# Kernel tuning notes

Hardware: AMD Instinct MI355X
Metric: run time of the kernel (lower is better)

## Reference

```python
import jax, jax.numpy as jnp
import numpy as np

EPS = 1e-6

def setup_inputs() -> dict:
    key = jax.random.key(0)
    k1, k2 = jax.random.split(key)
    N, B, T, D = 12, 4, 2048, 768
    layer_outputs = jax.random.normal(k1, (N, B, T, D), dtype=jnp.float32)
    pseudo_query = jax.random.normal(k2, (D,), dtype=jnp.float32) * 0.02
    key_norm_weight = jnp.ones((D,), dtype=jnp.float32)
    return {"layer_outputs": layer_outputs, "pseudo_query": pseudo_query,
            "key_norm_weight": key_norm_weight}

def reference(layer_outputs, pseudo_query, key_norm_weight):
    # layer_outputs: [N, B, T, D] (stacked V)
    V = layer_outputs
    # RMSNorm over last dim with learned scale
    inv_rms = jax.lax.rsqrt(jnp.mean(V * V, axis=-1, keepdims=True) + EPS)
    K = V * inv_rms * key_norm_weight  # [N,B,T,D]
    logits = jnp.einsum('d,nbtd->nbt', pseudo_query, K)  # [N,B,T]
    alpha = jax.nn.softmax(logits, axis=0)               # softmax over layer dim
    h = jnp.einsum('nbt,nbtd->btd', alpha, V)            # [B,T,D]
    return h
```

## Files before the change

### kernel.cpp

```cpp
#include <hip/hip_runtime.h>
#include <math.h>


constexpr int N_LAYERS = 12;
constexpr int D = 768;
constexpr int THREADS = 192;
constexpr float EPS = 1e-6f;

template<int CTRL>
__device__ __forceinline__ float dpp_add(float x) {
    int y = __builtin_amdgcn_update_dpp(0, __builtin_bit_cast(int, x),
                                        CTRL, 0xf, 0xf, false);
    return x + __builtin_bit_cast(float, y);
}

__device__ __forceinline__ float wave_sum_uniform(float x) {
    x = dpp_add<0x111>(x);
    x = dpp_add<0x112>(x);
    x = dpp_add<0x114>(x);
    x = dpp_add<0x118>(x);
    x = dpp_add<0x142>(x);
    x = dpp_add<0x143>(x);
    return __builtin_bit_cast(float,
        __builtin_amdgcn_readlane(__builtin_bit_cast(int, x), 63));
}

__global__ __launch_bounds__(THREADS)
void attnres_fused_kernel(const float* __restrict__ V,
                          const float* __restrict__ q,
                          const float* __restrict__ w,
                          float* __restrict__ out,
                          int BT)
{
    const int bt   = blockIdx.x;
    const int tid  = threadIdx.x;
    const int lane = tid & 63;
    const int wave = tid >> 6;

    const int d0 = tid * 4;
    float4 q4 = *reinterpret_cast<const float4*>(q + d0);
    float4 w4 = *reinterpret_cast<const float4*>(w + d0);
    float4 qw = make_float4(q4.x * w4.x, q4.y * w4.y, q4.z * w4.z, q4.w * w4.w);

    const size_t stride_n = (size_t)BT * (size_t)D;
    const float* base = V + (size_t)bt * (size_t)D + d0;

    float4 v[N_LAYERS];
    #pragma unroll
    for (int n = 0; n < N_LAYERS; ++n) {
        v[n] = *reinterpret_cast<const float4*>(base + (size_t)n * stride_n);
    }

    float ss[N_LAYERS], dq[N_LAYERS];
    #pragma unroll
    for (int n = 0; n < N_LAYERS; ++n) {
        float4 x = v[n];
        ss[n] = x.x * x.x + x.y * x.y + x.z * x.z + x.w * x.w;
        dq[n] = qw.x * x.x + qw.y * x.y + qw.z * x.z + qw.w * x.w;
    }

    float wred[2 * N_LAYERS];
    #pragma unroll
    for (int n = 0; n < N_LAYERS; ++n) {
        wred[n]            = wave_sum_uniform(ss[n]);
        wred[N_LAYERS + n] = wave_sum_uniform(dq[n]);
    }

    __shared__ float red[3][2 * N_LAYERS];
    if (lane == 0) {
        #pragma unroll
        for (int i = 0; i < 6; ++i) {
            *reinterpret_cast<float4*>(&red[wave][i * 4]) =
                make_float4(wred[i * 4 + 0], wred[i * 4 + 1],
                            wred[i * 4 + 2], wred[i * 4 + 3]);
        }
    }
    __syncthreads();

    float tot[2 * N_LAYERS];
    #pragma unroll
    for (int i = 0; i < 6; ++i) {
        float4 a = *reinterpret_cast<const float4*>(&red[0][i * 4]);
        float4 b = *reinterpret_cast<const float4*>(&red[1][i * 4]);
        float4 c = *reinterpret_cast<const float4*>(&red[2][i * 4]);
        tot[i * 4 + 0] = a.x + b.x + c.x;
        tot[i * 4 + 1] = a.y + b.y + c.y;
        tot[i * 4 + 2] = a.z + b.z + c.z;
        tot[i * 4 + 3] = a.w + b.w + c.w;
    }

    float logits[N_LAYERS];
    float mx = -3.0e38f;
    #pragma unroll
    for (int n = 0; n < N_LAYERS; ++n) {
        float inv_rms = rsqrtf(tot[n] * (1.0f / (float)D) + EPS);
        logits[n] = tot[N_LAYERS + n] * inv_rms;
        mx = fmaxf(mx, logits[n]);
    }
    float alpha[N_LAYERS];
    float sum = 0.0f;
    #pragma unroll
    for (int n = 0; n < N_LAYERS; ++n) {
        alpha[n] = __expf(logits[n] - mx);
        sum += alpha[n];
    }
    const float inv_sum = 1.0f / sum;

    float4 h = make_float4(0.f, 0.f, 0.f, 0.f);
    #pragma unroll
    for (int n = 0; n < N_LAYERS; ++n) {
        float a = alpha[n] * inv_sum;
        h.x += a * v[n].x;
        h.y += a * v[n].y;
        h.z += a * v[n].z;
        h.w += a * v[n].w;
    }

    *reinterpret_cast<float4*>(out + (size_t)bt * (size_t)D + d0) = h;
}

extern "C" void kernel_launch(void* const* d_in, const int* in_sizes, int n_in,
                              void* d_out, int out_size, void* d_ws, size_t ws_size,
                              hipStream_t stream)
{
    const float* V = (const float*)d_in[0];
    const float* q = (const float*)d_in[1];
    const float* w = (const float*)d_in[2];
    float* out = (float*)d_out;

    const int BT = out_size / D;

    attnres_fused_kernel<<<dim3(BT), dim3(THREADS), 0, stream>>>(V, q, w, out, BT);
}
```

Before: 60.78 us.

## Process multiple rows per block with double-buffered loads and bf16 value stash

Each block now handles eight token rows, alternating two register buffers so the next row's global loads are issued before the current row's reductions and barrier. Values used for the final weighted sum are packed to bf16 to reduce register pressure from the double buffers. The cross-wave reduction uses a double-buffered shared array and a raw barrier. The cost is lower precision in the output accumulation and fewer blocks in flight.

```diff
diff --git a/kernel.cpp b/kernel.cpp
--- a/kernel.cpp
+++ b/kernel.cpp
@@ -2,9 +2,10 @@
 #include <math.h>
 
 
-constexpr int N_LAYERS = 12;
+constexpr int NL = 12;
 constexpr int D = 768;
 constexpr int THREADS = 192;
+constexpr int PER = 8;
 constexpr float EPS = 1e-6f;
 
 template<int CTRL>
@@ -13,110 +14,138 @@
                                         CTRL, 0xf, 0xf, false);
     return x + __builtin_bit_cast(float, y);
 }
-
-__device__ __forceinline__ float wave_sum_uniform(float x) {
+__device__ __forceinline__ float wave_sum63(float x) {
     x = dpp_add<0x111>(x);
     x = dpp_add<0x112>(x);
     x = dpp_add<0x114>(x);
     x = dpp_add<0x118>(x);
     x = dpp_add<0x142>(x);
     x = dpp_add<0x143>(x);
-    return __builtin_bit_cast(float,
-        __builtin_amdgcn_readlane(__builtin_bit_cast(int, x), 63));
+    return x;
+}
+
+__device__ __forceinline__ unsigned pack_bf16x2(float a, float b) {
+    unsigned ua = __builtin_bit_cast(unsigned, a);
+    unsigned ub = __builtin_bit_cast(unsigned, b);
+    return ((ua + 0x8000u) >> 16) | ((ub + 0x8000u) & 0xFFFF0000u);
 }
 
 __global__ __launch_bounds__(THREADS)
-void attnres_fused_kernel(const float* __restrict__ V,
-                          const float* __restrict__ q,
-                          const float* __restrict__ w,
-                          float* __restrict__ out,
-                          int BT)
+void attnres_kernel(const float* __restrict__ V,
+                    const float* __restrict__ q,
+                    const float* __restrict__ w,
+                    float* __restrict__ out,
+                    int BT)
 {
-    const int bt   = blockIdx.x;
     const int tid  = threadIdx.x;
     const int lane = tid & 63;
     const int wave = tid >> 6;
+    const int d0   = tid * 4;
+    const int bt_base = blockIdx.x * PER;
 
-    const int d0 = tid * 4;
     float4 q4 = *reinterpret_cast<const float4*>(q + d0);
     float4 w4 = *reinterpret_cast<const float4*>(w + d0);
-    float4 qw = make_float4(q4.x * w4.x, q4.y * w4.y, q4.z * w4.z, q4.w * w4.w);
+    const float4 qw = make_float4(q4.x * w4.x, q4.y * w4.y,
+                                  q4.z * w4.z, q4.w * w4.w);
 
     const size_t stride_n = (size_t)BT * (size_t)D;
-    const float* base = V + (size_t)bt * (size_t)D + d0;
 
-    float4 v[N_LAYERS];
-    #pragma unroll
-    for (int n = 0; n < N_LAYERS; ++n) {
-        v[n] = *reinterpret_cast<const float4*>(base + (size_t)n * stride_n);
+    __shared__ float red[2][3][2 * NL];
+
+    float4   vA[NL],      vB[NL];
+    float    ssA[NL],     ssB[NL];
+    float    dqA[NL],     dqB[NL];
+    unsigned cA[2 * NL],  cB[2 * NL];
+
+    auto load_rows = [&](float4 (&v)[NL], int bt) {
+        const int btc = bt < BT ? bt : BT - 1;
+        const float* base = V + (size_t)btc * (size_t)D + d0;
+        #pragma unroll
+        for (int n = 0; n < NL; ++n)
+            v[n] = *reinterpret_cast<const float4*>(base + (size_t)n * stride_n);
+    };
+
+    auto ssdq_pack = [&](const float4 (&v)[NL], float (&ss)[NL],
+                         float (&dq)[NL], unsigned (&c)[2 * NL]) {
+        #pragma unroll
+        for (int n = 0; n < NL; ++n) {
+            const float4 x = v[n];
+            ss[n] = x.x * x.x + x.y * x.y + x.z * x.z + x.w * x.w;
+            dq[n] = qw.x * x.x + qw.y * x.y + qw.z * x.z + qw.w * x.w;
+            c[2 * n + 0] = pack_bf16x2(x.x, x.y);
+            c[2 * n + 1] = pack_bf16x2(x.z, x.w);
+        }
+    };
+
+    auto finish = [&](float (&ss)[NL], float (&dq)[NL],
+                      const unsigned (&c)[2 * NL], int bt, int p) {
+        float r[2 * NL];
+        #pragma unroll
+        for (int n = 0; n < NL; ++n) {
+            r[n]      = wave_sum63(ss[n]);
+            r[NL + n] = wave_sum63(dq[n]);
+        }
+        if (lane == 63) {
+            #pragma unroll
+            for (int i6 = 0; i6 < 6; ++i6)
+                *reinterpret_cast<float4*>(&red[p][wave][4 * i6]) =
+                    make_float4(r[4 * i6 + 0], r[4 * i6 + 1],
+                                r[4 * i6 + 2], r[4 * i6 + 3]);
+        }
+        __builtin_amdgcn_sched_barrier(0);
+        asm volatile("s_waitcnt lgkmcnt(0)");
+        __builtin_amdgcn_s_barrier();
+        __builtin_amdgcn_sched_barrier(0);
+
+        float tot[2 * NL];
+        #pragma unroll
+        for (int i6 = 0; i6 < 6; ++i6) {
+            float4 a  = *reinterpret_cast<const float4*>(&red[p][0][4 * i6]);
+            float4 b  = *reinterpret_cast<const float4*>(&red[p][1][4 * i6]);
+            float4 cc = *reinterpret_cast<const float4*>(&red[p][2][4 * i6]);
+            tot[4 * i6 + 0] = a.x + b.x + cc.x;
+            tot[4 * i6 + 1] = a.y + b.y + cc.y;
+            tot[4 * i6 + 2] = a.z + b.z + cc.z;
+            tot[4 * i6 + 3] = a.w + b.w + cc.w;
+        }
+
+        float lg[NL], mx = -3.0e38f;
+        #pragma unroll
+        for (int n = 0; n < NL; ++n) {
+            const float ir = rsqrtf(tot[n] * (1.0f / (float)D) + EPS);
+            lg[n] = tot[NL + n] * ir;
+            mx = fmaxf(mx, lg[n]);
+        }
+        float al[NL], s = 0.0f;
+        #pragma unroll
+        for (int n = 0; n < NL; ++n) { al[n] = __expf(lg[n] - mx); s += al[n]; }
+        const float inv = 1.0f / s;
+
+        float4 h = make_float4(0.f, 0.f, 0.f, 0.f);
+        #pragma unroll
+        for (int n = 0; n < NL; ++n) {
+            const float a2 = al[n] * inv;
+            const unsigned c0 = c[2 * n + 0], c1 = c[2 * n + 1];
+            h.x += a2 * __builtin_bit_cast(float, c0 << 16);
+            h.y += a2 * __builtin_bit_cast(float, c0 & 0xFFFF0000u);
+            h.z += a2 * __builtin_bit_cast(float, c1 << 16);
+            h.w += a2 * __builtin_bit_cast(float, c1 & 0xFFFF0000u);
+        }
+        if (bt < BT)
+            *reinterpret_cast<float4*>(out + (size_t)bt * (size_t)D + d0) = h;
+    };
+
+    load_rows(vA, bt_base);
+    #pragma unroll 1
+    for (int i = 0; i < PER; i += 2) {
+        ssdq_pack(vA, ssA, dqA, cA);
+        load_rows(vB, bt_base + i + 1);
+        finish(ssA, dqA, cA, bt_base + i, 0);
+
+        ssdq_pack(vB, ssB, dqB, cB);
+        if (i + 2 < PER) load_rows(vA, bt_base + i + 2);
+        finish(ssB, dqB, cB, bt_base + i + 1, 1);
     }
-
-    float ss[N_LAYERS], dq[N_LAYERS];
-    #pragma unroll
-    for (int n = 0; n < N_LAYERS; ++n) {
-        float4 x = v[n];
-        ss[n] = x.x * x.x + x.y * x.y + x.z * x.z + x.w * x.w;
-        dq[n] = qw.x * x.x + qw.y * x.y + qw.z * x.z + qw.w * x.w;
-    }
-
-    float wred[2 * N_LAYERS];
-    #pragma unroll
-    for (int n = 0; n < N_LAYERS; ++n) {
-        wred[n]            = wave_sum_uniform(ss[n]);
-        wred[N_LAYERS + n] = wave_sum_uniform(dq[n]);
-    }
-
-    __shared__ float red[3][2 * N_LAYERS];
-    if (lane == 0) {
-        #pragma unroll
-        for (int i = 0; i < 6; ++i) {
-            *reinterpret_cast<float4*>(&red[wave][i * 4]) =
-                make_float4(wred[i * 4 + 0], wred[i * 4 + 1],
-                            wred[i * 4 + 2], wred[i * 4 + 3]);
-        }
-    }
-    __syncthreads();
-
-    float tot[2 * N_LAYERS];
-    #pragma unroll
-    for (int i = 0; i < 6; ++i) {
-        float4 a = *reinterpret_cast<const float4*>(&red[0][i * 4]);
-        float4 b = *reinterpret_cast<const float4*>(&red[1][i * 4]);
-        float4 c = *reinterpret_cast<const float4*>(&red[2][i * 4]);
-        tot[i * 4 + 0] = a.x + b.x + c.x;
-        tot[i * 4 + 1] = a.y + b.y + c.y;
-        tot[i * 4 + 2] = a.z + b.z + c.z;
-        tot[i * 4 + 3] = a.w + b.w + c.w;
-    }
-
-    float logits[N_LAYERS];
-    float mx = -3.0e38f;
-    #pragma unroll
-    for (int n = 0; n < N_LAYERS; ++n) {
-        float inv_rms = rsqrtf(tot[n] * (1.0f / (float)D) + EPS);
-        logits[n] = tot[N_LAYERS + n] * inv_rms;
-        mx = fmaxf(mx, logits[n]);
-    }
-    float alpha[N_LAYERS];
-    float sum = 0.0f;
-    #pragma unroll
-    for (int n = 0; n < N_LAYERS; ++n) {
-        alpha[n] = __expf(logits[n] - mx);
-        sum += alpha[n];
-    }
-    const float inv_sum = 1.0f / sum;
-
-    float4 h = make_float4(0.f, 0.f, 0.f, 0.f);
-    #pragma unroll
-    for (int n = 0; n < N_LAYERS; ++n) {
-        float a = alpha[n] * inv_sum;
-        h.x += a * v[n].x;
-        h.y += a * v[n].y;
-        h.z += a * v[n].z;
-        h.w += a * v[n].w;
-    }
-
-    *reinterpret_cast<float4*>(out + (size_t)bt * (size_t)D + d0) = h;
 }
 
 extern "C" void kernel_launch(void* const* d_in, const int* in_sizes, int n_in,
@@ -129,6 +158,7 @@
     float* out = (float*)d_out;
 
     const int BT = out_size / D;
+    const int blocks = (BT + PER - 1) / PER;
 
-    attnres_fused_kernel<<<dim3(BT), dim3(THREADS), 0, stream>>>(V, q, w, out, BT);
+    attnres_kernel<<<dim3(blocks), dim3(THREADS), 0, stream>>>(V, q, w, out, BT);
 }
```

New measurement: 77.47 us. 1.27x slower.
